# Performance work log

Hardware: AMD Instinct MI355X
Metric: run time of the kernel (lower is better)

## Reference

```python
import jax, jax.numpy as jnp
import numpy as np

R, T, D = 512, 512, 256   # robots, tasks, per-entity embedding dim
INPUT_DIM = 2 * D         # 512
HIDDEN_DIM = 512


def setup_inputs() -> dict:
    key = jax.random.key(0)
    k1, k2, k3, k4, k5, k6 = jax.random.split(key, 6)
    lim1 = 1.0 / np.sqrt(INPUT_DIM)
    lim2 = 1.0 / np.sqrt(HIDDEN_DIM)
    return {
        "robot_embeddings": jax.random.normal(k1, (R, D), dtype=jnp.float32),
        "task_embeddings": jax.random.normal(k2, (T, D), dtype=jnp.float32),
        "W1": jax.random.uniform(k3, (INPUT_DIM, HIDDEN_DIM), jnp.float32, -lim1, lim1),
        "b1": jax.random.uniform(k4, (HIDDEN_DIM,), jnp.float32, -lim1, lim1),
        "W2": jax.random.uniform(k5, (HIDDEN_DIM, 1), jnp.float32, -lim2, lim2),
        "b2": jax.random.uniform(k6, (1,), jnp.float32, -lim2, lim2),
    }


def reference(robot_embeddings, task_embeddings, W1, b1, W2, b2):
    # Equivalent to the nested loop: for each (robot, task) pair,
    # mlp(concat([robot, task])) -> scalar; output [R, T].
    # Split W1 into the robot half and the task half so we never
    # materialize the [R, T, 2D] concatenated tensor:
    #   concat(r, t) @ W1 == r @ W1[:D] + t @ W1[D:]
    rpart = robot_embeddings @ W1[:D]          # [R, H]
    tpart = task_embeddings @ W1[D:]           # [T, H]
    h = jax.nn.relu(rpart[:, None, :] + tpart[None, :, :] + b1)  # [R, T, H]
    scores = jnp.einsum("rth,ho->rt", h, W2) + b2[0]             # [R, T]
    return scores
```

## Files before the change

kernel.cpp:

```cpp
#include <hip/hip_runtime.h>
#include <hip/hip_fp16.h>


#define RT 512
#define DD 256
#define HD 512

typedef _Float16 h2 __attribute__((ext_vector_type(2)));
typedef _Float16 h8 __attribute__((ext_vector_type(8)));
typedef float f32x4 __attribute__((ext_vector_type(4)));

__device__ inline unsigned h2u(h2 v) { return __builtin_bit_cast(unsigned, v); }
__device__ inline h2 u2h(unsigned u) { return __builtin_bit_cast(h2, u); }
__device__ inline h2 pk(float a, float b) {
    return __builtin_bit_cast(h2, __builtin_amdgcn_cvt_pkrtz(a, b));
}

__global__ __launch_bounds__(256) void gemm_packed(
    const float* __restrict__ robot, const float* __restrict__ task,
    const float* __restrict__ W1, const float* __restrict__ b1,
    unsigned* __restrict__ wsu)
{
    __shared__ __attribute__((aligned(16))) unsigned smem[8192];
    unsigned short* Ws = (unsigned short*)smem;

    const int tid = threadIdx.x;
    const int wave = tid >> 6, lane = tid & 63;
    const int b = blockIdx.x;
    const int z = b >> 7, sub = b & 127;
    const int rtile = (sub & 15) * 32;
    const int htile = (sub >> 4) * 64;
    const float* X = z ? task : robot;
    const float* Wz = W1 + z * DD * HD;

    {
        const int hh = tid & 63, k0 = (tid >> 6) * 64;
        #pragma unroll
        for (int j = 0; j < 8; ++j) {
            float f[8];
            #pragma unroll
            for (int u = 0; u < 8; ++u)
                f[u] = Wz[(k0 + 8 * j + u) * HD + htile + hh];
            uint4 o = make_uint4(h2u(pk(f[0], f[1])), h2u(pk(f[2], f[3])),
                                 h2u(pk(f[4], f[5])), h2u(pk(f[6], f[7])));
            *(uint4*)((char*)Ws + ((hh * 512 + k0 * 2 + j * 16) ^ ((hh & 7) << 4))) = o;
        }
    }
    __syncthreads();

    const int wstrip = wave >> 1;
    const int wh = (wave & 1) * 32;
    const int lm = lane & 15;
    const int lkb = (lane >> 4) * 16;
    const int xrow = rtile + wstrip * 16 + lm;
    const float* Xp = &X[xrow * DD];

    f32x4 acc0 = {0.f, 0.f, 0.f, 0.f}, acc1 = {0.f, 0.f, 0.f, 0.f};
    #pragma unroll
    for (int ks = 0; ks < 8; ++ks) {
        const float* xp = Xp + ks * 32 + (lane >> 4) * 8;
        float4 v0 = *(const float4*)xp, v1 = *(const float4*)(xp + 4);
        uint4 bu = make_uint4(h2u(pk(v0.x, v0.y)), h2u(pk(v0.z, v0.w)),
                              h2u(pk(v1.x, v1.y)), h2u(pk(v1.z, v1.w)));
        h8 bb = __builtin_bit_cast(h8, bu);
        const int h0 = wh + lm, h1 = wh + 16 + lm;
        h8 a0 = *(const h8*)((const char*)Ws + ((h0 * 512 + ks * 64 + lkb) ^ ((h0 & 7) << 4)));
        h8 a1 = *(const h8*)((const char*)Ws + ((h1 * 512 + ks * 64 + lkb) ^ ((h1 & 7) << 4)));
        acc0 = __builtin_amdgcn_mfma_f32_16x16x32_f16(a0, bb, acc0, 0, 0, 0);
        acc1 = __builtin_amdgcn_mfma_f32_16x16x32_f16(a1, bb, acc1, 0, 0, 0);
    }

    unsigned* P = wsu + z * (256 * RT);
    const int r = xrow;
    #pragma unroll
    for (int mf = 0; mf < 2; ++mf) {
        f32x4 acc = mf ? acc1 : acc0;
        const int hq = htile + wh + mf * 16 + (lane >> 4) * 4;
        float4 bv = make_float4(0.f, 0.f, 0.f, 0.f);
        if (z == 0) bv = *(const float4*)&b1[hq];
        P[((hq >> 1) + 0) * RT + r] = h2u(pk(acc[0] + bv.x, acc[1] + bv.y));
        P[((hq >> 1) + 1) * RT + r] = h2u(pk(acc[2] + bv.z, acc[3] + bv.w));
    }
}

__global__ __launch_bounds__(512) void score(
    const unsigned* __restrict__ wsu, const float* __restrict__ W2,
    const float* __restrict__ b2, float* __restrict__ out)
{
    __shared__ __attribute__((aligned(16))) unsigned smem[16384];
    unsigned* rs = smem;
    unsigned* ts = smem + 8192;

    const unsigned* rpP = wsu;
    const unsigned* tpP = wsu + 256 * RT;
    const int tid = threadIdx.x;
    const int rbase = blockIdx.y * 32, tbase = blockIdx.x * 32;

    #pragma unroll
    for (int i = 0; i < 8; ++i) {
        int u = tid + 512 * i;
        int hp = (u >> 3) & 255, rq = (u & 7) * 4;
        if (u < 2048)
            *(uint4*)&rs[hp * 32 + rq] = *(const uint4*)&rpP[hp * RT + rbase + rq];
        else
            *(uint4*)&ts[hp * 32 + rq] = *(const uint4*)&tpP[hp * RT + tbase + rq];
    }
    __syncthreads();

    const int wave = tid >> 6, lane = tid & 63;
    const int ly = (lane >> 3) & 7, lx = lane & 7;
    const h2 hzero = {};
    float acc[4][4] = {};
    const int s0 = wave * 32;
    #pragma unroll 4
    for (int s = s0; s < s0 + 32; ++s) {
        uint4 da = *(const uint4*)&rs[s * 32 + 4 * ly];
        uint4 dc = *(const uint4*)&ts[s * 32 + 4 * lx];
        float2 wf = *(const float2*)&W2[2 * s];
        h2 wv = pk(wf.x, wf.y);
        h2 a[4] = {u2h(da.x), u2h(da.y), u2h(da.z), u2h(da.w)};
        h2 c[4] = {u2h(dc.x), u2h(dc.y), u2h(dc.z), u2h(dc.w)};
        #pragma unroll
        for (int i2 = 0; i2 < 4; ++i2)
            #pragma unroll
            for (int j2 = 0; j2 < 4; ++j2) {
                h2 p = a[i2] + c[j2];
                p = __builtin_elementwise_max(p, hzero);
                acc[i2][j2] = __builtin_amdgcn_fdot2(p, wv, acc[i2][j2], false);
            }
    }

    __syncthreads();
    float* red = (float*)smem;
    {
        float* p = &red[wave * 1280 + lane * 20];
        #pragma unroll
        for (int i2 = 0; i2 < 4; ++i2)
            *(float4*)&p[4 * i2] = make_float4(acc[i2][0], acc[i2][1], acc[i2][2], acc[i2][3]);
    }
    __syncthreads();
    const float b2v = b2[0];
    #pragma unroll
    for (int half = 0; half < 2; ++half) {
        int j = tid + half * 512;
        float sum = 0.f;
        #pragma unroll
        for (int w = 0; w < 8; ++w) sum += red[w * 1280 + (j >> 4) * 20 + (j & 15)];
        int ly2 = j >> 7, lx2 = (j >> 4) & 7, dr = (j >> 2) & 3, dt = j & 3;
        out[(rbase + 4 * ly2 + dr) * RT + tbase + 4 * lx2 + dt] = sum + b2v;
    }
}

extern "C" void kernel_launch(void* const* d_in, const int* in_sizes, int n_in,
                              void* d_out, int out_size, void* d_ws, size_t ws_size,
                              hipStream_t stream) {
    const float* robot = (const float*)d_in[0];
    const float* task  = (const float*)d_in[1];
    const float* W1    = (const float*)d_in[2];
    const float* b1    = (const float*)d_in[3];
    const float* W2    = (const float*)d_in[4];
    const float* b2    = (const float*)d_in[5];
    float* out = (float*)d_out;
    unsigned* wsu = (unsigned*)d_ws;

    gemm_packed<<<dim3(256), 256, 0, stream>>>(robot, task, W1, b1, wsu);
    score<<<dim3(16, 16), 512, 0, stream>>>(wsu, W2, b2, out);
}
```

Baseline: 18.97 us.

## Fuse projection GEMM into score kernel, recomputing per-tile projections

Merges the two kernels into one. Each 32x32 output block now computes its own robot and task projections with MFMA, in hidden-dim chunks of 64, staging fp16 W1 through LDS. The next chunk of W1 is prefetched into registers while the current one is used. This removes the second launch and the workspace round trip through global memory. The cost is heavy redundant GEMM work: each block recomputes projections that are shared across 16 blocks. It also adds two barriers per chunk and uses a large LDS footprint (72KB), which limits occupancy.

Result: slower. 32.83 us (+73.0%).

```diff
diff --git a/kernel.cpp b/kernel.cpp
--- a/kernel.cpp
+++ b/kernel.cpp
@@ -15,119 +15,121 @@
 __device__ inline h2 pk(float a, float b) {
     return __builtin_bit_cast(h2, __builtin_amdgcn_cvt_pkrtz(a, b));
 }
+__device__ inline unsigned pku(float a, float b) { return h2u(pk(a, b)); }
 
-__global__ __launch_bounds__(256) void gemm_packed(
+__global__ __launch_bounds__(512) void fused(
     const float* __restrict__ robot, const float* __restrict__ task,
     const float* __restrict__ W1, const float* __restrict__ b1,
-    unsigned* __restrict__ wsu)
+    const float* __restrict__ W2, const float* __restrict__ b2,
+    float* __restrict__ out)
 {
-    __shared__ __attribute__((aligned(16))) unsigned smem[8192];
-    unsigned short* Ws = (unsigned short*)smem;
+    __shared__ __attribute__((aligned(16))) unsigned char smem[73728];
+    unsigned* rs = (unsigned*)(smem + 65536);
+    unsigned* ts = (unsigned*)(smem + 69632);
 
     const int tid = threadIdx.x;
     const int wave = tid >> 6, lane = tid & 63;
-    const int b = blockIdx.x;
-    const int z = b >> 7, sub = b & 127;
-    const int rtile = (sub & 15) * 32;
-    const int htile = (sub >> 4) * 64;
-    const float* X = z ? task : robot;
-    const float* Wz = W1 + z * DD * HD;
+    const int rbase = blockIdx.y * 32, tbase = blockIdx.x * 32;
 
-    {
-        const int hh = tid & 63, k0 = (tid >> 6) * 64;
+    const int wz = wave & 1;
+    const int hstrip = wave >> 1;
+    const int lm = lane & 15, lq = lane >> 4;
+
+    const float* X = wz ? task : robot;
+    const int xbase = wz ? tbase : rbase;
+    uint4 breg[2][8];
+    #pragma unroll
+    for (int f = 0; f < 2; ++f) {
+        const float* xp = &X[(xbase + f * 16 + lm) * DD + lq * 8];
         #pragma unroll
-        for (int j = 0; j < 8; ++j) {
-            float f[8];
-            #pragma unroll
-            for (int u = 0; u < 8; ++u)
-                f[u] = Wz[(k0 + 8 * j + u) * HD + htile + hh];
-            uint4 o = make_uint4(h2u(pk(f[0], f[1])), h2u(pk(f[2], f[3])),
-                                 h2u(pk(f[4], f[5])), h2u(pk(f[6], f[7])));
-            *(uint4*)((char*)Ws + ((hh * 512 + k0 * 2 + j * 16) ^ ((hh & 7) << 4))) = o;
+        for (int ks = 0; ks < 8; ++ks) {
+            float4 p0 = *(const float4*)(xp + ks * 32);
+            float4 p1 = *(const float4*)(xp + ks * 32 + 4);
+            breg[f][ks] = make_uint4(pku(p0.x, p0.y), pku(p0.z, p0.w),
+                                     pku(p1.x, p1.y), pku(p1.z, p1.w));
         }
     }
-    __syncthreads();
 
-    const int wstrip = wave >> 1;
-    const int wh = (wave & 1) * 32;
-    const int lm = lane & 15;
-    const int lkb = (lane >> 4) * 16;
-    const int xrow = rtile + wstrip * 16 + lm;
-    const float* Xp = &X[xrow * DD];
+    const int hq = tid & 15;
+    const int kg = tid >> 4;
+    float4 wreg[2][8];
+    #pragma unroll
+    for (int z = 0; z < 2; ++z)
+        #pragma unroll
+        for (int u = 0; u < 8; ++u)
+            wreg[z][u] = *(const float4*)&W1[(z * DD + kg * 8 + u) * HD + hq * 4];
 
-    f32x4 acc0 = {0.f, 0.f, 0.f, 0.f}, acc1 = {0.f, 0.f, 0.f, 0.f};
-    #pragma unroll
-    for (int ks = 0; ks < 8; ++ks) {
-        const float* xp = Xp + ks * 32 + (lane >> 4) * 8;
-        float4 v0 = *(const float4*)xp, v1 = *(const float4*)(xp + 4);
-        uint4 bu = make_uint4(h2u(pk(v0.x, v0.y)), h2u(pk(v0.z, v0.w)),
-                              h2u(pk(v1.x, v1.y)), h2u(pk(v1.z, v1.w)));
-        h8 bb = __builtin_bit_cast(h8, bu);
-        const int h0 = wh + lm, h1 = wh + 16 + lm;
-        h8 a0 = *(const h8*)((const char*)Ws + ((h0 * 512 + ks * 64 + lkb) ^ ((h0 & 7) << 4)));
-        h8 a1 = *(const h8*)((const char*)Ws + ((h1 * 512 + ks * 64 + lkb) ^ ((h1 & 7) << 4)));
-        acc0 = __builtin_amdgcn_mfma_f32_16x16x32_f16(a0, bb, acc0, 0, 0, 0);
-        acc1 = __builtin_amdgcn_mfma_f32_16x16x32_f16(a1, bb, acc1, 0, 0, 0);
-    }
-
-    unsigned* P = wsu + z * (256 * RT);
-    const int r = xrow;
-    #pragma unroll
-    for (int mf = 0; mf < 2; ++mf) {
-        f32x4 acc = mf ? acc1 : acc0;
-        const int hq = htile + wh + mf * 16 + (lane >> 4) * 4;
-        float4 bv = make_float4(0.f, 0.f, 0.f, 0.f);
-        if (z == 0) bv = *(const float4*)&b1[hq];
-        P[((hq >> 1) + 0) * RT + r] = h2u(pk(acc[0] + bv.x, acc[1] + bv.y));
-        P[((hq >> 1) + 1) * RT + r] = h2u(pk(acc[2] + bv.z, acc[3] + bv.w));
-    }
-}
-
-__global__ __launch_bounds__(512) void score(
-    const unsigned* __restrict__ wsu, const float* __restrict__ W2,
-    const float* __restrict__ b2, float* __restrict__ out)
-{
-    __shared__ __attribute__((aligned(16))) unsigned smem[16384];
-    unsigned* rs = smem;
-    unsigned* ts = smem + 8192;
-
-    const unsigned* rpP = wsu;
-    const unsigned* tpP = wsu + 256 * RT;
-    const int tid = threadIdx.x;
-    const int rbase = blockIdx.y * 32, tbase = blockIdx.x * 32;
-
-    #pragma unroll
-    for (int i = 0; i < 8; ++i) {
-        int u = tid + 512 * i;
-        int hp = (u >> 3) & 255, rq = (u & 7) * 4;
-        if (u < 2048)
-            *(uint4*)&rs[hp * 32 + rq] = *(const uint4*)&rpP[hp * RT + rbase + rq];
-        else
-            *(uint4*)&ts[hp * 32 + rq] = *(const uint4*)&tpP[hp * RT + tbase + rq];
-    }
-    __syncthreads();
-
-    const int wave = tid >> 6, lane = tid & 63;
+    float sacc[4][4] = {};
     const int ly = (lane >> 3) & 7, lx = lane & 7;
     const h2 hzero = {};
-    float acc[4][4] = {};
-    const int s0 = wave * 32;
-    #pragma unroll 4
-    for (int s = s0; s < s0 + 32; ++s) {
-        uint4 da = *(const uint4*)&rs[s * 32 + 4 * ly];
-        uint4 dc = *(const uint4*)&ts[s * 32 + 4 * lx];
-        float2 wf = *(const float2*)&W2[2 * s];
-        h2 wv = pk(wf.x, wf.y);
-        h2 a[4] = {u2h(da.x), u2h(da.y), u2h(da.z), u2h(da.w)};
-        h2 c[4] = {u2h(dc.x), u2h(dc.y), u2h(dc.z), u2h(dc.w)};
+
+    #pragma unroll 1
+    for (int it = 0; it < 8; ++it) {
+        const int hc = it * 64;
+
         #pragma unroll
-        for (int i2 = 0; i2 < 4; ++i2)
+        for (int z = 0; z < 2; ++z) {
+            const float4 w0 = wreg[z][0], w1 = wreg[z][1], w2v = wreg[z][2], w3 = wreg[z][3];
+            const float4 w4 = wreg[z][4], w5 = wreg[z][5], w6 = wreg[z][6], w7 = wreg[z][7];
+            #define STG(HH2, C) { \
+                int h = hq * 4 + HH2; \
+                uint4 o = make_uint4(pku(w0.C, w1.C), pku(w2v.C, w3.C), \
+                                     pku(w4.C, w5.C), pku(w6.C, w7.C)); \
+                *(uint4*)(smem + z * 32768 + ((h * 512 + kg * 16) ^ ((h & 7) << 4))) = o; }
+            STG(0, x) STG(1, y) STG(2, z) STG(3, w)
+            #undef STG
+        }
+        if (it < 7) {
+            const int hcn = hc + 64;
             #pragma unroll
-            for (int j2 = 0; j2 < 4; ++j2) {
-                h2 p = a[i2] + c[j2];
-                p = __builtin_elementwise_max(p, hzero);
-                acc[i2][j2] = __builtin_amdgcn_fdot2(p, wv, acc[i2][j2], false);
-            }
+            for (int z = 0; z < 2; ++z)
+                #pragma unroll
+                for (int u = 0; u < 8; ++u)
+                    wreg[z][u] = *(const float4*)&W1[(z * DD + kg * 8 + u) * HD + hcn + hq * 4];
+        }
+        __syncthreads();
+
+        f32x4 acc0 = {0.f, 0.f, 0.f, 0.f}, acc1 = {0.f, 0.f, 0.f, 0.f};
+        const int h0 = hstrip * 16;
+        #pragma unroll
+        for (int ks = 0; ks < 8; ++ks) {
+            int ha = h0 + lm;
+            h8 a = *(const h8*)(smem + wz * 32768 +
+                                ((ha * 512 + ks * 64 + lq * 16) ^ ((ha & 7) << 4)));
+            acc0 = __builtin_amdgcn_mfma_f32_16x16x32_f16(a, __builtin_bit_cast(h8, breg[0][ks]), acc0, 0, 0, 0);
+            acc1 = __builtin_amdgcn_mfma_f32_16x16x32_f16(a, __builtin_bit_cast(h8, breg[1][ks]), acc1, 0, 0, 0);
+        }
+        {
+            const int hloc = h0 + lq * 4;
+            float4 bv = make_float4(0.f, 0.f, 0.f, 0.f);
+            if (wz == 0) bv = *(const float4*)&b1[hc + hloc];
+            unsigned* dst = wz ? ts : rs;
+            const int hp = hloc >> 1;
+            dst[(hp + 0) * 32 + lm]      = pku(acc0[0] + bv.x, acc0[1] + bv.y);
+            dst[(hp + 1) * 32 + lm]      = pku(acc0[2] + bv.z, acc0[3] + bv.w);
+            dst[(hp + 0) * 32 + 16 + lm] = pku(acc1[0] + bv.x, acc1[1] + bv.y);
+            dst[(hp + 1) * 32 + 16 + lm] = pku(acc1[2] + bv.z, acc1[3] + bv.w);
+        }
+        __syncthreads();
+
+        #pragma unroll
+        for (int q = 0; q < 4; ++q) {
+            int s = wave * 4 + q;
+            uint4 da = *(const uint4*)&rs[s * 32 + 4 * ly];
+            uint4 dc = *(const uint4*)&ts[s * 32 + 4 * lx];
+            float2 wf = *(const float2*)&W2[2 * (it * 32 + s)];
+            h2 wv = pk(wf.x, wf.y);
+            h2 aa[4] = {u2h(da.x), u2h(da.y), u2h(da.z), u2h(da.w)};
+            h2 cc[4] = {u2h(dc.x), u2h(dc.y), u2h(dc.z), u2h(dc.w)};
+            #pragma unroll
+            for (int i2 = 0; i2 < 4; ++i2)
+                #pragma unroll
+                for (int j2 = 0; j2 < 4; ++j2) {
+                    h2 p = aa[i2] + cc[j2];
+                    p = __builtin_elementwise_max(p, hzero);
+                    sacc[i2][j2] = __builtin_amdgcn_fdot2(p, wv, sacc[i2][j2], false);
+                }
+        }
     }
 
     __syncthreads();
@@ -136,7 +138,7 @@
         float* p = &red[wave * 1280 + lane * 20];
         #pragma unroll
         for (int i2 = 0; i2 < 4; ++i2)
-            *(float4*)&p[4 * i2] = make_float4(acc[i2][0], acc[i2][1], acc[i2][2], acc[i2][3]);
+            *(float4*)&p[4 * i2] = make_float4(sacc[i2][0], sacc[i2][1], sacc[i2][2], sacc[i2][3]);
     }
     __syncthreads();
     const float b2v = b2[0];
@@ -161,8 +163,7 @@
     const float* W2    = (const float*)d_in[4];
     const float* b2    = (const float*)d_in[5];
     float* out = (float*)d_out;
-    unsigned* wsu = (unsigned*)d_ws;
+    (void)d_ws; (void)ws_size;
 
-    gemm_packed<<<dim3(256), 256, 0, stream>>>(robot, task, W1, b1, wsu);
-    score<<<dim3(16, 16), 512, 0, stream>>>(wsu, W2, b2, out);
+    fused<<<dim3(16, 16), 512, 0, stream>>>(robot, task, W1, b1, W2, b2, out);
 }
```
